# Performance work log

Hardware: AMD Instinct MI355X
Metric: run time of the kernel (lower is better)

Reference implementation:

```python
import jax, jax.numpy as jnp
import numpy as np

KSZ = 3      # kernel_size
NH = 4       # num_heads


def setup_inputs() -> dict:
    key = jax.random.key(0)
    ks = jax.random.split(key, 4)
    B, D, H, W, C = 1, 28, 28, 28, 192
    N = D * H * W
    s = 0.02  # trunc_normal std used by the module's init
    return {
        "x": jax.random.normal(ks[0], (B, N, C), jnp.float32),
        "Wq": jax.random.normal(ks[1], (C, C), jnp.float32) * s,
        "bq": jnp.zeros((C,), jnp.float32),
        "Wkv": jax.random.normal(ks[2], (C, 2 * C), jnp.float32) * s,
        "bkv": jnp.zeros((2 * C,), jnp.float32),
        "Wp": jax.random.normal(ks[3], (C, C), jnp.float32) * s,
        "bp": jnp.zeros((C,), jnp.float32),
        "D": D, "H": H, "W": W,
    }


def _windows(t, D, H, W):
    # t: (B, D+2, H+2, W+2, nh, hc) zero-padded; gather the 27 neighborhood
    # offsets (same flattening order as unfold: d-major, then h, then w).
    return jnp.stack(
        [t[:, dz:dz + D, dy:dy + H, dx:dx + W]
         for dz in range(KSZ) for dy in range(KSZ) for dx in range(KSZ)],
        axis=4)  # (B, D, H, W, 27, nh, hc)


def reference(x, Wq, bq, Wkv, bkv, Wp, bp, D, H, W):
    B, N, C = x.shape
    hc = C // NH
    scale = hc ** (-0.5)
    xv = x.reshape(B, D, H, W, C)

    q = (xv @ Wq + bq).reshape(B, D, H, W, NH, hc) * scale
    kv = (xv @ Wkv + bkv).reshape(B, D, H, W, 2, NH, hc)
    k, v = kv[..., 0, :, :], kv[..., 1, :, :]

    pad = ((0, 0), (1, 1), (1, 1), (1, 1), (0, 0), (0, 0))
    kwin = _windows(jnp.pad(k, pad), D, H, W)  # (B,D,H,W,27,nh,hc)
    vwin = _windows(jnp.pad(v, pad), D, H, W)

    # per-voxel 1x27 attention over the 3x3x3 neighborhood
    attn = jnp.einsum('bdhwnc,bdhwknc->bdhwnk', q, kwin)
    attn = jax.nn.softmax(attn, axis=-1)
    out = jnp.einsum('bdhwnk,bdhwknc->bdhwnc', attn, vwin)
    out = out.reshape(B, D, H, W, C) @ Wp + bp
    return out.reshape(B, N, C)
```

## Files before the change

kernel.cpp:

```cpp
#include <hip/hip_runtime.h>
#include <math.h>

#define CDIM 192
#define DD 28
#define NVOX (DD * DD * DD)

typedef __attribute__((ext_vector_type(8))) short bf16x8;
typedef __attribute__((ext_vector_type(4))) float f32x4;

__device__ __forceinline__ float blo(unsigned int u) {
  union { unsigned int i; float f; } w; w.i = u << 16; return w.f;
}
__device__ __forceinline__ float bhi(unsigned int u) {
  union { unsigned int i; float f; } w; w.i = u & 0xffff0000u; return w.f;
}
__device__ __forceinline__ unsigned short f2bf(float f) {
  union { float ff; unsigned int i; } w; w.ff = f;
  unsigned int x = w.i;
  return (unsigned short)((x + 0x7fffu + ((x >> 16) & 1u)) >> 16);
}

__global__ __launch_bounds__(256) void prep_w(
    const float* __restrict__ Wq, const float* __restrict__ Wkv,
    const float* __restrict__ Wp, const float* __restrict__ bq,
    const float* __restrict__ bkv,
    unsigned short* __restrict__ WqkvT, unsigned short* __restrict__ WpT,
    float* __restrict__ biasAll, float scale)
{
  int t = blockIdx.x * 256 + threadIdx.x;
  if (t < 576 * CDIM) {
    const int n = t / CDIM, k = t % CDIM;
    const float v = (n < CDIM) ? Wq[k * CDIM + n] * scale
                               : Wkv[k * 2 * CDIM + (n - CDIM)];
    WqkvT[t] = f2bf(v);
    return;
  }
  t -= 576 * CDIM;
  if (t < CDIM * CDIM) {
    const int n = t / CDIM, k = t % CDIM;
    WpT[t] = f2bf(Wp[k * CDIM + n]);
    return;
  }
  t -= CDIM * CDIM;
  if (t < 576)
    biasAll[t] = (t < CDIM) ? bq[t] * scale : bkv[t - CDIM];
}

__global__ __launch_bounds__(256) void gemm_qkv(
    const float* __restrict__ X,
    const unsigned short* __restrict__ Bt,
    const float* __restrict__ biasAll,
    unsigned short* __restrict__ qb,
    unsigned short* __restrict__ kvb)
{
  __shared__ unsigned short As[64 * 200];
  __shared__ unsigned short Bs[64 * 200];
  const int tid = threadIdx.x;
  const int m0 = blockIdx.x * 64;
  const int by = blockIdx.y;

#pragma unroll
  for (int u = tid; u < 1536; u += 256) {
    const int row = u / 24, c = (u % 24) * 8;
    const float4 f0 = *(const float4*)(&X[(size_t)(m0 + row) * CDIM + c]);
    const float4 f1 = *(const float4*)(&X[(size_t)(m0 + row) * CDIM + c + 4]);
    unsigned short o[8] = {f2bf(f0.x), f2bf(f0.y), f2bf(f0.z), f2bf(f0.w),
                           f2bf(f1.x), f2bf(f1.y), f2bf(f1.z), f2bf(f1.w)};
    *(uint4*)(&As[row * 200 + c]) = *(const uint4*)o;
  }

  const int l = tid & 63, w = tid >> 6;
  const int wm = (w >> 1) * 32, wn = (w & 1) * 32;
  const int lr = l & 15, lk = (l >> 4) * 8;
  const unsigned short* pa = &As[(wm + lr) * 200 + lk];
  const unsigned short* pb = &Bs[(wn + lr) * 200 + lk];

  for (int nt = by; nt < 9; nt += 2) {
    const int n0 = nt * 64;
    __syncthreads();
#pragma unroll
    for (int u = tid; u < 1536; u += 256) {
      const int row = u / 24, c = (u % 24) * 8;
      *(uint4*)(&Bs[row * 200 + c]) =
          *(const uint4*)(&Bt[(size_t)(n0 + row) * CDIM + c]);
    }
    __syncthreads();

    f32x4 acc[2][2] = {};
#pragma unroll
    for (int k0 = 0; k0 < CDIM; k0 += 32) {
      const bf16x8 a0 = *(const bf16x8*)(pa + k0);
      const bf16x8 a1 = *(const bf16x8*)(pa + 16 * 200 + k0);
      const bf16x8 b0 = *(const bf16x8*)(pb + k0);
      const bf16x8 b1 = *(const bf16x8*)(pb + 16 * 200 + k0);
      acc[0][0] = __builtin_amdgcn_mfma_f32_16x16x32_bf16(a0, b0, acc[0][0], 0, 0, 0);
      acc[0][1] = __builtin_amdgcn_mfma_f32_16x16x32_bf16(a0, b1, acc[0][1], 0, 0, 0);
      acc[1][0] = __builtin_amdgcn_mfma_f32_16x16x32_bf16(a1, b0, acc[1][0], 0, 0, 0);
      acc[1][1] = __builtin_amdgcn_mfma_f32_16x16x32_bf16(a1, b1, acc[1][1], 0, 0, 0);
    }

#pragma unroll
    for (int i = 0; i < 2; ++i)
#pragma unroll
      for (int j = 0; j < 2; ++j) {
        const int gc = n0 + wn + j * 16 + lr;
        const float bv = biasAll[gc];
#pragma unroll
        for (int r = 0; r < 4; ++r) {
          const int gr = m0 + wm + i * 16 + (l >> 4) * 4 + r;
          const float v = acc[i][j][r] + bv;
          if (gc < CDIM)
            qb[(size_t)gr * CDIM + gc] = f2bf(v);
          else
            kvb[(size_t)gr * 2 * CDIM + (gc - CDIM)] = f2bf(v);
        }
      }
  }
}

__device__ __forceinline__ void load_row(const unsigned short* rp,
    uint4& K0, uint4& K1, uint4& K2, uint4& V0, uint4& V1, uint4& V2) {
  const uint4* kp = (const uint4*)rp;
  const uint4* vp = (const uint4*)(rp + CDIM);
  K0 = kp[0]; K1 = kp[1]; K2 = kp[2];
  V0 = vp[0]; V1 = vp[1]; V2 = vp[2];
}

__device__ __forceinline__ void do_row(
    uint4 K0, uint4 K1, uint4 K2, uint4 V0, uint4 V1, uint4 V2,
    const float* __restrict__ qf, float* __restrict__ out,
    float& m, float& s, int lm1, int lp1, bool okm, bool okp) {
  const unsigned int ku[12] = {K0.x, K0.y, K0.z, K0.w, K1.x, K1.y, K1.z, K1.w,
                               K2.x, K2.y, K2.z, K2.w};
  const unsigned int vu[12] = {V0.x, V0.y, V0.z, V0.w, V1.x, V1.y, V1.z, V1.w,
                               V2.x, V2.y, V2.z, V2.w};
  float p0 = 0.f, p1 = 0.f, p2 = 0.f;
#pragma unroll
  for (int i = 0; i < 12; ++i) {
    p1 += qf[2*i] * blo(ku[i]) + qf[2*i+1] * bhi(ku[i]);
    unsigned int t = (unsigned int)__shfl((int)ku[i], lm1);
    p0 += qf[2*i] * blo(t) + qf[2*i+1] * bhi(t);
    t = (unsigned int)__shfl((int)ku[i], lp1);
    p2 += qf[2*i] * blo(t) + qf[2*i+1] * bhi(t);
  }
  p0 += __shfl_xor(p0, 32);
  p1 += __shfl_xor(p1, 32);
  p2 += __shfl_xor(p2, 32);
  const float l0 = okm ? p0 : -INFINITY;
  const float l2 = okp ? p2 : -INFINITY;
  const float nm = fmaxf(m, fmaxf(p1, fmaxf(l0, l2)));
  const float sc = __expf(m - nm);
  const float w0 = okm ? __expf(p0 - nm) : 0.f;
  const float w1 = __expf(p1 - nm);
  const float w2 = okp ? __expf(p2 - nm) : 0.f;
  s = s * sc + w0 + w1 + w2;
  m = nm;
#pragma unroll
  for (int i = 0; i < 12; ++i) {
    const unsigned int am = (unsigned int)__shfl((int)vu[i], lm1);
    const unsigned int ap = (unsigned int)__shfl((int)vu[i], lp1);
    out[2*i]   = out[2*i]   * sc + w0 * blo(am) + w1 * blo(vu[i]) + w2 * blo(ap);
    out[2*i+1] = out[2*i+1] * sc + w0 * bhi(am) + w1 * bhi(vu[i]) + w2 * bhi(ap);
  }
}

__global__ __launch_bounds__(256) void attn3d_line(
    const unsigned short* __restrict__ q,
    const unsigned short* __restrict__ kv,
    unsigned short* __restrict__ y)
{
  const int bid = blockIdx.x;
  const int zy = (bid & 7) * 98 + (bid >> 3);
  const int z = zy / 28, yr = zy % 28;
  const int h = threadIdx.x >> 6;
  const int lane = threadIdx.x & 63;
  const int x = lane & 31;
  const int g = lane >> 5;
  const int xc = x < 28 ? x : 27;
  const int cb = h * 48 + g * 24;
  const int vox = (z * 28 + yr) * 28 + xc;

  float qf[24];
  {
    const uint4* qp = (const uint4*)(q + (size_t)vox * CDIM + cb);
    const uint4 a = qp[0], b = qp[1], c = qp[2];
    const unsigned int uu[12] = {a.x, a.y, a.z, a.w, b.x, b.y, b.z, b.w,
                                 c.x, c.y, c.z, c.w};
#pragma unroll
    for (int i = 0; i < 12; ++i) { qf[2*i] = blo(uu[i]); qf[2*i+1] = bhi(uu[i]); }
  }

  const int nx = 3 - (x == 0) - (x == 27);
  const int nyv = 3 - (yr == 0) - (yr == 27);
  const int nzv = 3 - (z == 0) - (z == 27);
  const int noob = 27 - nx * nyv * nzv;
  float m = noob ? 0.f : -INFINITY;
  float s = (float)noob;
  float out[24];
#pragma unroll
  for (int i = 0; i < 24; ++i) out[i] = 0.f;

  const int lm1 = lane - 1, lp1 = lane + 1;
  const bool okm = (x > 0), okp = (x < 27);

  const unsigned short* rbase = kv + (size_t)xc * 384 + cb;
  const int zm = z > 0 ? z - 1 : 0,  zp = z < 27 ? z + 1 : 27;
  const int ym = yr > 0 ? yr - 1 : 0, yp = yr < 27 ? yr + 1 : 27;
  const int r0 = (zm*28+ym)*10752, r1 = (zm*28+yr)*10752, r2 = (zm*28+yp)*10752;
  const int r3 = (z *28+ym)*10752, r4 = (z *28+yr)*10752, r5 = (z *28+yp)*10752;
  const int r6 = (zp*28+ym)*10752, r7 = (zp*28+yr)*10752, r8 = (zp*28+yp)*10752;
  const bool vz0 = z > 0, vz2 = z < 27, vy0 = yr > 0, vy2 = yr < 27;
  const bool v0 = vz0 && vy0, v1 = vz0, v2 = vz0 && vy2;
  const bool v3 = vy0,                  v5 = vy2;
  const bool v6 = vz2 && vy0, v7 = vz2, v8 = vz2 && vy2;

  uint4 Ak0, Ak1, Ak2, Av0, Av1, Av2;
  uint4 Bk0, Bk1, Bk2, Bv0, Bv1, Bv2;

  load_row(rbase + r0, Ak0, Ak1, Ak2, Av0, Av1, Av2);
  load_row(rbase + r1, Bk0, Bk1, Bk2, Bv0, Bv1, Bv2);
  if (v0) do_row(Ak0, Ak1, Ak2, Av0, Av1, Av2, qf, out, m, s, lm1, lp1, okm, okp);
  load_row(rbase + r2, Ak0, Ak1, Ak2, Av0, Av1, Av2);
  if (v1) do_row(Bk0, Bk1, Bk2, Bv0, Bv1, Bv2, qf, out, m, s, lm1, lp1, okm, okp);
  load_row(rbase + r3, Bk0, Bk1, Bk2, Bv0, Bv1, Bv2);
  if (v2) do_row(Ak0, Ak1, Ak2, Av0, Av1, Av2, qf, out, m, s, lm1, lp1, okm, okp);
  load_row(rbase + r4, Ak0, Ak1, Ak2, Av0, Av1, Av2);
  if (v3) do_row(Bk0, Bk1, Bk2, Bv0, Bv1, Bv2, qf, out, m, s, lm1, lp1, okm, okp);
  load_row(rbase + r5, Bk0, Bk1, Bk2, Bv0, Bv1, Bv2);
  do_row(Ak0, Ak1, Ak2, Av0, Av1, Av2, qf, out, m, s, lm1, lp1, okm, okp);
  load_row(rbase + r6, Ak0, Ak1, Ak2, Av0, Av1, Av2);
  if (v5) do_row(Bk0, Bk1, Bk2, Bv0, Bv1, Bv2, qf, out, m, s, lm1, lp1, okm, okp);
  load_row(rbase + r7, Bk0, Bk1, Bk2, Bv0, Bv1, Bv2);
  if (v6) do_row(Ak0, Ak1, Ak2, Av0, Av1, Av2, qf, out, m, s, lm1, lp1, okm, okp);
  load_row(rbase + r8, Ak0, Ak1, Ak2, Av0, Av1, Av2);
  if (v7) do_row(Bk0, Bk1, Bk2, Bv0, Bv1, Bv2, qf, out, m, s, lm1, lp1, okm, okp);
  if (v8) do_row(Ak0, Ak1, Ak2, Av0, Av1, Av2, qf, out, m, s, lm1, lp1, okm, okp);

  if (x < 28) {
    const float inv = 1.f / s;
    unsigned int ou[12];
#pragma unroll
    for (int i = 0; i < 12; ++i)
      ou[i] = (unsigned int)f2bf(out[2*i] * inv) |
              ((unsigned int)f2bf(out[2*i+1] * inv) << 16);
    uint4* yp = (uint4*)(y + (size_t)vox * CDIM + cb);
    yp[0] = make_uint4(ou[0], ou[1], ou[2], ou[3]);
    yp[1] = make_uint4(ou[4], ou[5], ou[6], ou[7]);
    yp[2] = make_uint4(ou[8], ou[9], ou[10], ou[11]);
  }
}

__global__ __launch_bounds__(256) void gemm_out(
    const unsigned short* __restrict__ A,
    const unsigned short* __restrict__ Bt,
    const float* __restrict__ bias,
    float* __restrict__ C)
{
  __shared__ unsigned short As[64 * 200];
  __shared__ unsigned short Bs[64 * 200];
  const int tid = threadIdx.x;
  const int n0 = blockIdx.x * 64;
  const int m0 = blockIdx.y * 64;

#pragma unroll
  for (int u = tid; u < 1536; u += 256) {
    const int row = u / 24, c = (u % 24) * 8;
    *(uint4*)(&As[row * 200 + c]) =
        *(const uint4*)(&A[(size_t)(m0 + row) * CDIM + c]);
    *(uint4*)(&Bs[row * 200 + c]) =
        *(const uint4*)(&Bt[(size_t)(n0 + row) * CDIM + c]);
  }
  __syncthreads();

  const int l = tid & 63, w = tid >> 6;
  const int wm = (w >> 1) * 32, wn = (w & 1) * 32;
  const int lr = l & 15, lk = (l >> 4) * 8;

  f32x4 acc[2][2] = {};
  const unsigned short* pa = &As[(wm + lr) * 200 + lk];
  const unsigned short* pb = &Bs[(wn + lr) * 200 + lk];

#pragma unroll
  for (int k0 = 0; k0 < CDIM; k0 += 32) {
    const bf16x8 a0 = *(const bf16x8*)(pa + k0);
    const bf16x8 a1 = *(const bf16x8*)(pa + 16 * 200 + k0);
    const bf16x8 b0 = *(const bf16x8*)(pb + k0);
    const bf16x8 b1 = *(const bf16x8*)(pb + 16 * 200 + k0);
    acc[0][0] = __builtin_amdgcn_mfma_f32_16x16x32_bf16(a0, b0, acc[0][0], 0, 0, 0);
    acc[0][1] = __builtin_amdgcn_mfma_f32_16x16x32_bf16(a0, b1, acc[0][1], 0, 0, 0);
    acc[1][0] = __builtin_amdgcn_mfma_f32_16x16x32_bf16(a1, b0, acc[1][0], 0, 0, 0);
    acc[1][1] = __builtin_amdgcn_mfma_f32_16x16x32_bf16(a1, b1, acc[1][1], 0, 0, 0);
  }

#pragma unroll
  for (int i = 0; i < 2; ++i)
#pragma unroll
    for (int j = 0; j < 2; ++j) {
      const int gc = n0 + wn + j * 16 + lr;
      const float bv = bias[gc];
#pragma unroll
      for (int r = 0; r < 4; ++r) {
        const int gr = m0 + wm + i * 16 + (l >> 4) * 4 + r;
        C[(size_t)gr * CDIM + gc] = acc[i][j][r] + bv;
      }
    }
}

extern "C" void kernel_launch(void* const* d_in, const int* in_sizes, int n_in,
                              void* d_out, int out_size, void* d_ws, size_t ws_size,
                              hipStream_t stream) {
  const float* x   = (const float*)d_in[0];
  const float* Wq  = (const float*)d_in[1];
  const float* bq  = (const float*)d_in[2];
  const float* Wkv = (const float*)d_in[3];
  const float* bkv = (const float*)d_in[4];
  const float* Wp  = (const float*)d_in[5];
  const float* bp  = (const float*)d_in[6];
  float* out = (float*)d_out;

  unsigned short* WqkvT = (unsigned short*)d_ws;
  unsigned short* WpT   = WqkvT + 576 * CDIM;
  float*          biasA = (float*)(WpT + CDIM * CDIM);
  unsigned short* qb    = (unsigned short*)(biasA + 576);
  unsigned short* kvb   = qb + (size_t)NVOX * CDIM;
  unsigned short* yb    = kvb + (size_t)NVOX * 2 * CDIM;

  const float scale = 1.0f / sqrtf(48.0f);

  prep_w<<<(148032 + 255) / 256, 256, 0, stream>>>(
      Wq, Wkv, Wp, bq, bkv, WqkvT, WpT, biasA, scale);

  gemm_qkv<<<dim3(NVOX / 64, 2), 256, 0, stream>>>(x, WqkvT, biasA, qb, kvb);
  attn3d_line<<<DD * DD, 256, 0, stream>>>(qb, kvb, yb);
  gemm_out<<<dim3(3, NVOX / 64), 256, 0, stream>>>(yb, WpT, bp, out);
}
```

Before: 146.9 us.

## Split QKV GEMM over all N-tiles and load neighbor K/V directly instead of shuffling

The QKV GEMM grid grows from 2 to 9 column blocks, so each block computes a single 64-wide N tile and loads A and B together, with one barrier. The X-to-bf16 conversion now uses a packed float2-to-bf162 intrinsic. The attention kernel drops the cross-lane shuffles used to fetch x-1/x+1 neighbors and issues separate global loads for those neighbor rows inside a loop over dz/dy, replacing the hand-unrolled double-buffered schedule. The trade-off: every block re-reads and re-converts the X tile, the attention kernel issues three times the K/V loads (mostly cache hits), and the manual load/compute overlap is gone.

Result: slower. 190.5 us (+29.7%).

```diff
diff --git a/kernel.cpp b/kernel.cpp
--- a/kernel.cpp
+++ b/kernel.cpp
@@ -1,4 +1,5 @@
 #include <hip/hip_runtime.h>
+#include <hip/hip_bf16.h>
 #include <math.h>
 
 #define CDIM 192
@@ -18,6 +19,10 @@
   union { float ff; unsigned int i; } w; w.ff = f;
   unsigned int x = w.i;
   return (unsigned short)((x + 0x7fffu + ((x >> 16) & 1u)) >> 16);
+}
+__device__ __forceinline__ unsigned int pk2(float lo, float hi) {
+  __hip_bfloat162 h = __float22bfloat162_rn(make_float2(lo, hi));
+  union { __hip_bfloat162 h2; unsigned int u; } cv; cv.h2 = h; return cv.u;
 }
 
 __global__ __launch_bounds__(256) void prep_w(
@@ -57,17 +62,20 @@
   __shared__ unsigned short Bs[64 * 200];
   const int tid = threadIdx.x;
   const int m0 = blockIdx.x * 64;
-  const int by = blockIdx.y;
+  const int n0 = blockIdx.y * 64;
 
 #pragma unroll
   for (int u = tid; u < 1536; u += 256) {
     const int row = u / 24, c = (u % 24) * 8;
     const float4 f0 = *(const float4*)(&X[(size_t)(m0 + row) * CDIM + c]);
     const float4 f1 = *(const float4*)(&X[(size_t)(m0 + row) * CDIM + c + 4]);
-    unsigned short o[8] = {f2bf(f0.x), f2bf(f0.y), f2bf(f0.z), f2bf(f0.w),
-                           f2bf(f1.x), f2bf(f1.y), f2bf(f1.z), f2bf(f1.w)};
+    unsigned int o[4] = {pk2(f0.x, f0.y), pk2(f0.z, f0.w),
+                         pk2(f1.x, f1.y), pk2(f1.z, f1.w)};
     *(uint4*)(&As[row * 200 + c]) = *(const uint4*)o;
-  }
+    *(uint4*)(&Bs[row * 200 + c]) =
+        *(const uint4*)(&Bt[(size_t)(n0 + row) * CDIM + c]);
+  }
+  __syncthreads();
 
   const int l = tid & 63, w = tid >> 6;
   const int wm = (w >> 1) * 32, wn = (w & 1) * 32;
@@ -75,93 +83,35 @@
   const unsigned short* pa = &As[(wm + lr) * 200 + lk];
   const unsigned short* pb = &Bs[(wn + lr) * 200 + lk];
 
-  for (int nt = by; nt < 9; nt += 2) {
-    const int n0 = nt * 64;
-    __syncthreads();
-#pragma unroll
-    for (int u = tid; u < 1536; u += 256) {
-      const int row = u / 24, c = (u % 24) * 8;
-      *(uint4*)(&Bs[row * 200 + c]) =
-          *(const uint4*)(&Bt[(size_t)(n0 + row) * CDIM + c]);
+  f32x4 acc[2][2] = {};
+#pragma unroll
+  for (int k0 = 0; k0 < CDIM; k0 += 32) {
+    const bf16x8 a0 = *(const bf16x8*)(pa + k0);
+    const bf16x8 a1 = *(const bf16x8*)(pa + 16 * 200 + k0);
+    const bf16x8 b0 = *(const bf16x8*)(pb + k0);
+    const bf16x8 b1 = *(const bf16x8*)(pb + 16 * 200 + k0);
+    acc[0][0] = __builtin_amdgcn_mfma_f32_16x16x32_bf16(a0, b0, acc[0][0], 0, 0, 0);
+    acc[0][1] = __builtin_amdgcn_mfma_f32_16x16x32_bf16(a0, b1, acc[0][1], 0, 0, 0);
+    acc[1][0] = __builtin_amdgcn_mfma_f32_16x16x32_bf16(a1, b0, acc[1][0], 0, 0, 0);
+    acc[1][1] = __builtin_amdgcn_mfma_f32_16x16x32_bf16(a1, b1, acc[1][1], 0, 0, 0);
+  }
+
+#pragma unroll
+  for (int i = 0; i < 2; ++i)
+#pragma unroll
+    for (int j = 0; j < 2; ++j) {
+      const int gc = n0 + wn + j * 16 + lr;
+      const float bv = biasAll[gc];
+#pragma unroll
+      for (int r = 0; r < 4; ++r) {
+        const int gr = m0 + wm + i * 16 + (l >> 4) * 4 + r;
+        const float v = acc[i][j][r] + bv;
+        if (gc < CDIM)
+          qb[(size_t)gr * CDIM + gc] = f2bf(v);
+        else
+          kvb[(size_t)gr * 2 * CDIM + (gc - CDIM)] = f2bf(v);
+      }
     }
-    __syncthreads();
-
-    f32x4 acc[2][2] = {};
-#pragma unroll
-    for (int k0 = 0; k0 < CDIM; k0 += 32) {
-      const bf16x8 a0 = *(const bf16x8*)(pa + k0);
-      const bf16x8 a1 = *(const bf16x8*)(pa + 16 * 200 + k0);
-      const bf16x8 b0 = *(const bf16x8*)(pb + k0);
-      const bf16x8 b1 = *(const bf16x8*)(pb + 16 * 200 + k0);
-      acc[0][0] = __builtin_amdgcn_mfma_f32_16x16x32_bf16(a0, b0, acc[0][0], 0, 0, 0);
-      acc[0][1] = __builtin_amdgcn_mfma_f32_16x16x32_bf16(a0, b1, acc[0][1], 0, 0, 0);
-      acc[1][0] = __builtin_amdgcn_mfma_f32_16x16x32_bf16(a1, b0, acc[1][0], 0, 0, 0);
-      acc[1][1] = __builtin_amdgcn_mfma_f32_16x16x32_bf16(a1, b1, acc[1][1], 0, 0, 0);
-    }
-
-#pragma unroll
-    for (int i = 0; i < 2; ++i)
-#pragma unroll
-      for (int j = 0; j < 2; ++j) {
-        const int gc = n0 + wn + j * 16 + lr;
-        const float bv = biasAll[gc];
-#pragma unroll
-        for (int r = 0; r < 4; ++r) {
-          const int gr = m0 + wm + i * 16 + (l >> 4) * 4 + r;
-          const float v = acc[i][j][r] + bv;
-          if (gc < CDIM)
-            qb[(size_t)gr * CDIM + gc] = f2bf(v);
-          else
-            kvb[(size_t)gr * 2 * CDIM + (gc - CDIM)] = f2bf(v);
-        }
-      }
-  }
-}
-
-__device__ __forceinline__ void load_row(const unsigned short* rp,
-    uint4& K0, uint4& K1, uint4& K2, uint4& V0, uint4& V1, uint4& V2) {
-  const uint4* kp = (const uint4*)rp;
-  const uint4* vp = (const uint4*)(rp + CDIM);
-  K0 = kp[0]; K1 = kp[1]; K2 = kp[2];
-  V0 = vp[0]; V1 = vp[1]; V2 = vp[2];
-}
-
-__device__ __forceinline__ void do_row(
-    uint4 K0, uint4 K1, uint4 K2, uint4 V0, uint4 V1, uint4 V2,
-    const float* __restrict__ qf, float* __restrict__ out,
-    float& m, float& s, int lm1, int lp1, bool okm, bool okp) {
-  const unsigned int ku[12] = {K0.x, K0.y, K0.z, K0.w, K1.x, K1.y, K1.z, K1.w,
-                               K2.x, K2.y, K2.z, K2.w};
-  const unsigned int vu[12] = {V0.x, V0.y, V0.z, V0.w, V1.x, V1.y, V1.z, V1.w,
-                               V2.x, V2.y, V2.z, V2.w};
-  float p0 = 0.f, p1 = 0.f, p2 = 0.f;
-#pragma unroll
-  for (int i = 0; i < 12; ++i) {
-    p1 += qf[2*i] * blo(ku[i]) + qf[2*i+1] * bhi(ku[i]);
-    unsigned int t = (unsigned int)__shfl((int)ku[i], lm1);
-    p0 += qf[2*i] * blo(t) + qf[2*i+1] * bhi(t);
-    t = (unsigned int)__shfl((int)ku[i], lp1);
-    p2 += qf[2*i] * blo(t) + qf[2*i+1] * bhi(t);
-  }
-  p0 += __shfl_xor(p0, 32);
-  p1 += __shfl_xor(p1, 32);
-  p2 += __shfl_xor(p2, 32);
-  const float l0 = okm ? p0 : -INFINITY;
-  const float l2 = okp ? p2 : -INFINITY;
-  const float nm = fmaxf(m, fmaxf(p1, fmaxf(l0, l2)));
-  const float sc = __expf(m - nm);
-  const float w0 = okm ? __expf(p0 - nm) : 0.f;
-  const float w1 = __expf(p1 - nm);
-  const float w2 = okp ? __expf(p2 - nm) : 0.f;
-  s = s * sc + w0 + w1 + w2;
-  m = nm;
-#pragma unroll
-  for (int i = 0; i < 12; ++i) {
-    const unsigned int am = (unsigned int)__shfl((int)vu[i], lm1);
-    const unsigned int ap = (unsigned int)__shfl((int)vu[i], lp1);
-    out[2*i]   = out[2*i]   * sc + w0 * blo(am) + w1 * blo(vu[i]) + w2 * blo(ap);
-    out[2*i+1] = out[2*i+1] * sc + w0 * bhi(am) + w1 * bhi(vu[i]) + w2 * bhi(ap);
-  }
 }
 
 __global__ __launch_bounds__(256) void attn3d_line(
@@ -175,8 +125,8 @@
   const int h = threadIdx.x >> 6;
   const int lane = threadIdx.x & 63;
   const int x = lane & 31;
+  const int xc = x < 28 ? x : 27;
   const int g = lane >> 5;
-  const int xc = x < 28 ? x : 27;
   const int cb = h * 48 + g * 24;
   const int vox = (z * 28 + yr) * 28 + xc;
 
@@ -200,41 +150,74 @@
 #pragma unroll
   for (int i = 0; i < 24; ++i) out[i] = 0.f;
 
-  const int lm1 = lane - 1, lp1 = lane + 1;
   const bool okm = (x > 0), okp = (x < 27);
-
-  const unsigned short* rbase = kv + (size_t)xc * 384 + cb;
-  const int zm = z > 0 ? z - 1 : 0,  zp = z < 27 ? z + 1 : 27;
-  const int ym = yr > 0 ? yr - 1 : 0, yp = yr < 27 ? yr + 1 : 27;
-  const int r0 = (zm*28+ym)*10752, r1 = (zm*28+yr)*10752, r2 = (zm*28+yp)*10752;
-  const int r3 = (z *28+ym)*10752, r4 = (z *28+yr)*10752, r5 = (z *28+yp)*10752;
-  const int r6 = (zp*28+ym)*10752, r7 = (zp*28+yr)*10752, r8 = (zp*28+yp)*10752;
-  const bool vz0 = z > 0, vz2 = z < 27, vy0 = yr > 0, vy2 = yr < 27;
-  const bool v0 = vz0 && vy0, v1 = vz0, v2 = vz0 && vy2;
-  const bool v3 = vy0,                  v5 = vy2;
-  const bool v6 = vz2 && vy0, v7 = vz2, v8 = vz2 && vy2;
-
-  uint4 Ak0, Ak1, Ak2, Av0, Av1, Av2;
-  uint4 Bk0, Bk1, Bk2, Bv0, Bv1, Bv2;
-
-  load_row(rbase + r0, Ak0, Ak1, Ak2, Av0, Av1, Av2);
-  load_row(rbase + r1, Bk0, Bk1, Bk2, Bv0, Bv1, Bv2);
-  if (v0) do_row(Ak0, Ak1, Ak2, Av0, Av1, Av2, qf, out, m, s, lm1, lp1, okm, okp);
-  load_row(rbase + r2, Ak0, Ak1, Ak2, Av0, Av1, Av2);
-  if (v1) do_row(Bk0, Bk1, Bk2, Bv0, Bv1, Bv2, qf, out, m, s, lm1, lp1, okm, okp);
-  load_row(rbase + r3, Bk0, Bk1, Bk2, Bv0, Bv1, Bv2);
-  if (v2) do_row(Ak0, Ak1, Ak2, Av0, Av1, Av2, qf, out, m, s, lm1, lp1, okm, okp);
-  load_row(rbase + r4, Ak0, Ak1, Ak2, Av0, Av1, Av2);
-  if (v3) do_row(Bk0, Bk1, Bk2, Bv0, Bv1, Bv2, qf, out, m, s, lm1, lp1, okm, okp);
-  load_row(rbase + r5, Bk0, Bk1, Bk2, Bv0, Bv1, Bv2);
-  do_row(Ak0, Ak1, Ak2, Av0, Av1, Av2, qf, out, m, s, lm1, lp1, okm, okp);
-  load_row(rbase + r6, Ak0, Ak1, Ak2, Av0, Av1, Av2);
-  if (v5) do_row(Bk0, Bk1, Bk2, Bv0, Bv1, Bv2, qf, out, m, s, lm1, lp1, okm, okp);
-  load_row(rbase + r7, Bk0, Bk1, Bk2, Bv0, Bv1, Bv2);
-  if (v6) do_row(Ak0, Ak1, Ak2, Av0, Av1, Av2, qf, out, m, s, lm1, lp1, okm, okp);
-  load_row(rbase + r8, Ak0, Ak1, Ak2, Av0, Av1, Av2);
-  if (v7) do_row(Bk0, Bk1, Bk2, Bv0, Bv1, Bv2, qf, out, m, s, lm1, lp1, okm, okp);
-  if (v8) do_row(Ak0, Ak1, Ak2, Av0, Av1, Av2, qf, out, m, s, lm1, lp1, okm, okp);
+  const int xm = okm ? xc - 1 : 0;
+  const int xp = okp ? xc + 1 : 27;
+  const size_t om = (size_t)xm * 384 + cb;
+  const size_t oc = (size_t)xc * 384 + cb;
+  const size_t op = (size_t)xp * 384 + cb;
+
+  for (int dz = -1; dz <= 1; ++dz) {
+    const int zz = z + dz;
+    if ((unsigned)zz >= 28u) continue;
+    for (int dy = -1; dy <= 1; ++dy) {
+      const int yv = yr + dy;
+      if ((unsigned)yv >= 28u) continue;
+      const unsigned short* rp = kv + (size_t)((zz * 28 + yv) * 28) * 384;
+
+      const uint4* kmp = (const uint4*)(rp + om);
+      const uint4* kcp = (const uint4*)(rp + oc);
+      const uint4* kpp = (const uint4*)(rp + op);
+      const uint4 Km0 = kmp[0], Km1 = kmp[1], Km2 = kmp[2];
+      const uint4 Kc0 = kcp[0], Kc1 = kcp[1], Kc2 = kcp[2];
+      const uint4 Kp0 = kpp[0], Kp1 = kpp[1], Kp2 = kpp[2];
+      const uint4* vmp = (const uint4*)(rp + om + CDIM);
+      const uint4* vcp = (const uint4*)(rp + oc + CDIM);
+      const uint4* vpp = (const uint4*)(rp + op + CDIM);
+      const uint4 Vm0 = vmp[0], Vm1 = vmp[1], Vm2 = vmp[2];
+      const uint4 Vc0 = vcp[0], Vc1 = vcp[1], Vc2 = vcp[2];
+      const uint4 Vp0 = vpp[0], Vp1 = vpp[1], Vp2 = vpp[2];
+
+      const unsigned int km[12] = {Km0.x, Km0.y, Km0.z, Km0.w, Km1.x, Km1.y,
+                                   Km1.z, Km1.w, Km2.x, Km2.y, Km2.z, Km2.w};
+      const unsigned int kc[12] = {Kc0.x, Kc0.y, Kc0.z, Kc0.w, Kc1.x, Kc1.y,
+                                   Kc1.z, Kc1.w, Kc2.x, Kc2.y, Kc2.z, Kc2.w};
+      const unsigned int kp[12] = {Kp0.x, Kp0.y, Kp0.z, Kp0.w, Kp1.x, Kp1.y,
+                                   Kp1.z, Kp1.w, Kp2.x, Kp2.y, Kp2.z, Kp2.w};
+      float p0 = 0.f, p1 = 0.f, p2 = 0.f;
+#pragma unroll
+      for (int i = 0; i < 12; ++i) {
+        p0 += qf[2*i] * blo(km[i]) + qf[2*i+1] * bhi(km[i]);
+        p1 += qf[2*i] * blo(kc[i]) + qf[2*i+1] * bhi(kc[i]);
+        p2 += qf[2*i] * blo(kp[i]) + qf[2*i+1] * bhi(kp[i]);
+      }
+      p0 += __shfl_xor(p0, 32);
+      p1 += __shfl_xor(p1, 32);
+      p2 += __shfl_xor(p2, 32);
+
+      const float l0 = okm ? p0 : -INFINITY;
+      const float l2 = okp ? p2 : -INFINITY;
+      const float nm = fmaxf(m, fmaxf(p1, fmaxf(l0, l2)));
+      const float sc = __expf(m - nm);
+      const float w0 = okm ? __expf(p0 - nm) : 0.f;
+      const float w1 = __expf(p1 - nm);
+      const float w2 = okp ? __expf(p2 - nm) : 0.f;
+      s = s * sc + w0 + w1 + w2;
+      m = nm;
+
+      const unsigned int vm[12] = {Vm0.x, Vm0.y, Vm0.z, Vm0.w, Vm1.x, Vm1.y,
+                                   Vm1.z, Vm1.w, Vm2.x, Vm2.y, Vm2.z, Vm2.w};
+      const unsigned int vc[12] = {Vc0.x, Vc0.y, Vc0.z, Vc0.w, Vc1.x, Vc1.y,
+                                   Vc1.z, Vc1.w, Vc2.x, Vc2.y, Vc2.z, Vc2.w};
+      const unsigned int vp[12] = {Vp0.x, Vp0.y, Vp0.z, Vp0.w, Vp1.x, Vp1.y,
+                                   Vp1.z, Vp1.w, Vp2.x, Vp2.y, Vp2.z, Vp2.w};
+#pragma unroll
+      for (int i = 0; i < 12; ++i) {
+        out[2*i]   = out[2*i]   * sc + w0 * blo(vm[i]) + w1 * blo(vc[i]) + w2 * blo(vp[i]);
+        out[2*i+1] = out[2*i+1] * sc + w0 * bhi(vm[i]) + w1 * bhi(vc[i]) + w2 * bhi(vp[i]);
+      }
+    }
+  }
 
   if (x < 28) {
     const float inv = 1.f / s;
@@ -330,7 +313,7 @@
   prep_w<<<(148032 + 255) / 256, 256, 0, stream>>>(
       Wq, Wkv, Wp, bq, bkv, WqkvT, WpT, biasA, scale);
 
-  gemm_qkv<<<dim3(NVOX / 64, 2), 256, 0, stream>>>(x, WqkvT, biasA, qb, kvb);
+  gemm_qkv<<<dim3(NVOX / 64, 9), 256, 0, stream>>>(x, WqkvT, biasA, qb, kvb);
   attn3d_line<<<DD * DD, 256, 0, stream>>>(qb, kvb, yb);
   gemm_out<<<dim3(3, NVOX / 64), 256, 0, stream>>>(yb, WpT, bp, out);
 }
```
